# Kernel tuning notes

Measured on AMD Instinct MI355X. Metric: run time of the kernel, lower is better.

The kernel has to match this reference:

```python
import jax, jax.numpy as jnp
import numpy as np

K_NN = 3
EPS = 1e-8
MASK_THRESH = 0.5


def _three_nn_interpolate(pts, known, feats):
    """pts: (B,N,3), known: (B,M,3), feats: (B,M,C) -> (B,N,C).
    Squared-distance 3-NN + inverse-distance weighted interpolation
    (pointnet2 three_nn / three_interpolate semantics)."""
    # (B,N,M) squared euclidean distances
    d2 = (jnp.sum(pts * pts, -1)[:, :, None]
          + jnp.sum(known * known, -1)[:, None, :]
          - 2.0 * jnp.einsum('bnd,bmd->bnm', pts, known))
    neg_d, idx = jax.lax.top_k(-d2, K_NN)          # (B,N,3)
    dist = jnp.maximum(-neg_d, 0.0)                # squared dists, clamp fp error
    dist_recip = 1.0 / (dist + EPS)
    weight = dist_recip / jnp.sum(dist_recip, -1, keepdims=True)  # (B,N,3)
    b_idx = jnp.arange(pts.shape[0])[:, None, None]
    gathered = feats[b_idx, idx]                   # (B,N,3,C)
    return jnp.sum(weight[..., None] * gathered, axis=2)  # (B,N,C)


def setup_inputs() -> dict:
    key = jax.random.key(0)
    ks = jax.random.split(key, 10)
    B, N, C = 4, 8192, 32
    M2, M3, M4, Mm = 8192, 4096, 2048, 4096
    sc = 10.0  # spread coords over a realistic metric range
    return {
        'points_mean': jax.random.normal(ks[0], (B, N, 3)) * sc,
        'known2': jax.random.normal(ks[1], (B, M2, 3)) * sc,
        'feats2': jax.random.normal(ks[2], (B, M2, C)),
        'known3': jax.random.normal(ks[3], (B, M3, 3)) * sc,
        'feats3': jax.random.normal(ks[4], (B, M3, C)),
        'known4': jax.random.normal(ks[5], (B, M4, 3)) * sc,
        'feats4': jax.random.normal(ks[6], (B, M4, C)),
        'match_points': jax.random.normal(ks[7], (B, Mm, 3)) * sc,
        'w_fc': jax.random.normal(ks[8], (64, 96)) * 0.1,
        'w_cls': jax.random.normal(ks[9], (1, 64)) * 0.1,
    }


def reference(points_mean, known2, feats2, known3, feats3, known4, feats4,
              match_points, w_fc, w_cls):
    p0 = _three_nn_interpolate(points_mean, known2, feats2)  # (B,N,32)
    p1 = _three_nn_interpolate(points_mean, known3, feats3)
    p2 = _three_nn_interpolate(points_mean, known4, feats4)
    pointwise = jnp.concatenate([p0, p1, p2], axis=-1) @ w_fc.T  # (B,N,64)
    pred_hm = pointwise @ w_cls.T                                 # (B,N,1)
    # GT mask: min distance to match points < 0.5 m
    d2 = (jnp.sum(points_mean * points_mean, -1)[:, :, None]
          + jnp.sum(match_points * match_points, -1)[:, None, :]
          - 2.0 * jnp.einsum('bnd,bmd->bnm', points_mean, match_points))
    min_d = jnp.sqrt(jnp.maximum(jnp.min(d2, axis=-1), 0.0))      # (B,N)
    gt_hm = (min_d < MASK_THRESH).astype(jnp.float32)
    return pred_hm, gt_hm
```

## Files before the change

### kernel.cpp

```cpp
#include <hip/hip_runtime.h>

typedef unsigned int u32;
typedef unsigned long long u64;
typedef float f32x2 __attribute__((ext_vector_type(2)));

#define NB 4
#define NQ 8192
#define MARGIN 0.0625f
#define NBKT 4096

#define OFF_C0   0u
#define OFF_C1   524288u
#define OFF_C2   786432u
#define OFF_CMP  917504u
#define OFF_SKEY 1179648u
#define OFF_BOX  2031616u
#define WS_NEW2  2068480u
#define OFF_CM   917504u
#define WS_OLD   (512u*1024 + 256u*1024 + 128u*1024 + 512u*1024)

struct __align__(32) CP { f32x2 x, y, z, w; };
struct DM { double x, y, z, w; };

__device__ __forceinline__ f32x2 fma2(f32x2 a, f32x2 b, f32x2 c) {
  return __builtin_elementwise_fma(a, b, c);
}

__device__ __forceinline__ float wmaxf(float v) {
#pragma unroll
  for (int o = 32; o; o >>= 1) v = fmaxf(v, __shfl_xor(v, o));
  return v;
}
__device__ __forceinline__ float wminf(float v) {
#pragma unroll
  for (int o = 32; o; o >>= 1) v = fminf(v, __shfl_xor(v, o));
  return v;
}

__device__ __forceinline__ void lexins(double& e0d, double& e1d, double& e2d,
                                       int& e0i, int& e1i, int& e2i,
                                       double d, int i) {
  if (d < e2d || (d == e2d && i < e2i)) {
    if (d < e0d || (d == e0d && i < e0i)) {
      e2d = e1d; e2i = e1i; e1d = e0d; e1i = e0i; e0d = d; e0i = i;
    } else if (d < e1d || (d == e1d && i < e1i)) {
      e2d = e1d; e2i = e1i; e1d = d; e1i = i;
    } else {
      e2d = d; e2i = i;
    }
  }
}

__device__ __forceinline__ void ins4(float kv, u32 idx,
                                     float& k0, float& k1, float& k2, float& k3,
                                     u32& i0, u32& i1, u32& i2, u32& i3) {
  if (kv < k3) {
    bool lt0 = kv < k0, lt1 = kv < k1, lt2 = kv < k2;
    k3 = lt2 ? k2 : kv;               i3 = lt2 ? i2 : idx;
    k2 = lt2 ? (lt1 ? k1 : kv) : k2;  i2 = lt2 ? (lt1 ? i1 : idx) : i2;
    k1 = lt1 ? (lt0 ? k0 : kv) : k1;  i1 = lt1 ? (lt0 ? i0 : idx) : i1;
    k0 = lt0 ? kv : k0;               i0 = lt0 ? idx : i0;
  }
}

__device__ __forceinline__ u32 spread10(u32 v) {
  v &= 0x3FFu;
  v = (v | (v << 16)) & 0x030000FFu;
  v = (v | (v << 8))  & 0x0300F00Fu;
  v = (v | (v << 4))  & 0x030C30C3u;
  v = (v | (v << 2))  & 0x09249249u;
  return v;
}
__device__ __forceinline__ u32 morton30(float x, float y, float z) {
  int xi = (int)((x + 64.f) * 8.f);
  int yi = (int)((y + 64.f) * 8.f);
  int zi = (int)((z + 64.f) * 8.f);
  xi = min(max(xi, 0), 1023); yi = min(max(yi, 0), 1023); zi = min(max(zi, 0), 1023);
  return spread10((u32)xi) | (spread10((u32)yi) << 1) | (spread10((u32)zi) << 2);
}

__device__ __forceinline__ size_t skey_abase(int arr) {
  return (arr == 0) ? 0 : (arr == 1) ? 32768 : (arr == 2) ? 49152
        : (arr == 3) ? 57344 : 73728;
}

__global__ __launch_bounds__(1024) void prep_csort(
    const float* __restrict__ k2p, const float* __restrict__ k3p,
    const float* __restrict__ k4p, const float* __restrict__ mmp,
    const float* __restrict__ pts, u64* __restrict__ skey) {
  __shared__ u32 hist[NBKT];
  const int arr = blockIdx.x, b = blockIdx.y, tid = threadIdx.x;
  const float* src = (arr == 0) ? k2p : (arr == 1) ? k3p : (arr == 2) ? k4p
                      : (arr == 3) ? mmp : pts;
  const int n = (arr == 0) ? 8192 : (arr == 1) ? 4096 : (arr == 2) ? 2048
                 : (arr == 3) ? 4096 : 8192;
  const float* sb = src + (size_t)b * n * 3;
  u64* skb = skey + skey_abase(arr) + (size_t)b * n;

  for (int i = tid; i < NBKT; i += 1024) hist[i] = 0;
  __syncthreads();
  for (int i = tid; i < n; i += 1024) {
    u32 k = morton30(sb[3 * i], sb[3 * i + 1], sb[3 * i + 2]);
    atomicAdd(&hist[k >> 18], 1u);
  }
  __syncthreads();
  for (int d = 1; d < NBKT; d <<= 1) {
    for (int i = tid; i < NBKT / (2 * d); i += 1024) {
      int idx = (2 * i + 2) * d - 1;
      hist[idx] += hist[idx - d];
    }
    __syncthreads();
  }
  if (tid == 0) hist[NBKT - 1] = 0;
  __syncthreads();
  for (int d = NBKT >> 1; d >= 1; d >>= 1) {
    for (int i = tid; i < NBKT / (2 * d); i += 1024) {
      int idx = (2 * i + 2) * d - 1;
      u32 t = hist[idx - d];
      hist[idx - d] = hist[idx];
      hist[idx] += t;
    }
    __syncthreads();
  }
  for (int i = tid; i < n; i += 1024) {
    u32 k = morton30(sb[3 * i], sb[3 * i + 1], sb[3 * i + 2]);
    u32 pos = atomicAdd(&hist[k >> 18], 1u);
    skb[pos] = ((u64)k << 32) | (u32)i;
  }
}

__global__ __launch_bounds__(512) void refine_emit(
    const float* __restrict__ k2p, const float* __restrict__ k3p,
    const float* __restrict__ k4p, const float* __restrict__ mmp,
    const float* __restrict__ pts, u64* __restrict__ skey,
    CP* __restrict__ c0, CP* __restrict__ c1, CP* __restrict__ c2,
    CP* __restrict__ cmp, float* __restrict__ boxes) {
  __shared__ u64 ex[512];
  const int widx = blockIdx.x, b = blockIdx.y, tid = threadIdx.x;
  int arr, win;
  if (widx < 16)      { arr = 0; win = widx; }
  else if (widx < 24) { arr = 1; win = widx - 16; }
  else if (widx < 28) { arr = 2; win = widx - 24; }
  else if (widx < 36) { arr = 3; win = widx - 28; }
  else                { arr = 4; win = widx - 36; }
  const float* src = (arr == 0) ? k2p : (arr == 1) ? k3p : (arr == 2) ? k4p
                      : (arr == 3) ? mmp : pts;
  const int n = (arr == 0) ? 8192 : (arr == 1) ? 4096 : (arr == 2) ? 2048
                 : (arr == 3) ? 4096 : 8192;
  u64* skb = skey + skey_abase(arr) + (size_t)b * n;
  const int e = win * 512 + tid;
  u64 v = skb[e];

  for (int k = 2; k <= 512; k <<= 1) {
    for (int j = k >> 1; j > 0; j >>= 1) {
      u64 w;
      if (j < 64) {
        w = __shfl_xor(v, j);
      } else {
        __syncthreads();
        ex[tid] = v;
        __syncthreads();
        w = ex[tid ^ j];
      }
      bool up = (tid & k) == 0;
      bool lower = (tid & j) == 0;
      v = (up == lower) ? (v < w ? v : w) : (v < w ? w : v);
    }
  }
  skb[e] = v;
  if (arr == 4) return;

  u32 p = (u32)v;
  const float* sb = src + (size_t)b * n * 3;
  float x = sb[3 * p], y = sb[3 * p + 1], z = sb[3 * p + 2];
  {
    CP* dst = (arr == 0) ? c0 : (arr == 1) ? c1 : (arr == 2) ? c2 : cmp;
    float* df = (float*)(dst + (size_t)b * (n >> 1) + (e >> 1));
    int sl = e & 1;
    df[sl]     = x;
    df[2 + sl] = y;
    df[4 + sl] = z;
    df[6 + sl] = fmaf(z, z, fmaf(y, y, x * x));
  }
  float xlo = x, xhi = x, ylo = y, yhi = y, zlo = z, zhi = z;
#pragma unroll
  for (int off = 1; off < 64; off <<= 1) {
    xlo = fminf(xlo, __shfl_xor(xlo, off)); xhi = fmaxf(xhi, __shfl_xor(xhi, off));
    ylo = fminf(ylo, __shfl_xor(ylo, off)); yhi = fmaxf(yhi, __shfl_xor(yhi, off));
    zlo = fminf(zlo, __shfl_xor(zlo, off)); zhi = fmaxf(zhi, __shfl_xor(zhi, off));
  }
  if ((tid & 63) == 0) {
    const int nG = n >> 6, g = e >> 6;
    const int boff = (arr == 0) ? 0 : (arr == 1) ? 512 : (arr == 2) ? 768 : 896;
    float* bx = boxes + ((size_t)boff + (size_t)b * nG + g) * 8;
    bx[0] = xlo; bx[1] = xhi; bx[2] = ylo; bx[3] = yhi; bx[4] = zlo; bx[5] = zhi;
    bx[6] = 0.f; bx[7] = 0.f;
  }
}

__device__ __forceinline__ void scan_pairs16(
    const CP* __restrict__ cg, u32 ebase,
    f32x2 mx2, f32x2 my2, f32x2 mz2,
    float& k0, float& k1, float& k2, float& k3,
    u32& i0, u32& i1, u32& i2, u32& i3) {
#pragma unroll 4
  for (int gg = 0; gg < 16; gg += 4) {
    f32x2 key[4];
#pragma unroll
    for (int u = 0; u < 4; ++u) {
      CP c = cg[gg + u];
      key[u] = fma2(mx2, c.x, fma2(my2, c.y, fma2(mz2, c.z, c.w)));
    }
#pragma unroll
    for (int u = 0; u < 4; ++u) {
      float ka = key[u].x, kb = key[u].y;
      if (fminf(ka, kb) < k3) {
        u32 ib = ebase + (u32)((gg + u) * 2);
        ins4(ka, ib,     k0, k1, k2, k3, i0, i1, i2, i3);
        ins4(kb, ib + 1, k0, k1, k2, k3, i0, i1, i2, i3);
      }
    }
  }
}

struct Smem5 {
  float  qx[32], qy[32], qz[32];
  double qdx[32], qdy[32], qdz[32], qn[32];
  u32    oq[32];
  u32    di[3][32][4][4];
  double mmin[32][8];
  float  wv[96];
  float  wq[32][9];
  u32    iq[32][9];
  float  contrib[32][9];
  float4 stage[4][2][64];
};

__global__ __launch_bounds__(256, 4) void fused_sorted4(
    const float* __restrict__ pts,
    const float* __restrict__ f2, const float* __restrict__ f3,
    const float* __restrict__ f4,
    const float* __restrict__ wfc, const float* __restrict__ wcls,
    const CP* __restrict__ c0, const CP* __restrict__ c1,
    const CP* __restrict__ c2, const CP* __restrict__ cmp,
    const u64* __restrict__ skey, const float* __restrict__ boxes,
    float* __restrict__ out) {
  __shared__ Smem5 s;
  const int tid = threadIdx.x;
  const int b = blockIdx.y;
  const int tile = blockIdx.x;
  const int lane = tid & 63;
  const int q = tid & 31;
  const int h = (tid >> 5) & 1;
  const int wid = __builtin_amdgcn_readfirstlane(tid >> 6);

  if (tid < 32) {
    u64 kv = skey[73728 + (size_t)b * NQ + tile * 32 + tid];
    u32 p = (u32)kv;
    const float* pb = pts + (size_t)b * NQ * 3;
    float x = pb[3 * p], y = pb[3 * p + 1], z = pb[3 * p + 2];
    s.qx[tid] = x; s.qy[tid] = y; s.qz[tid] = z; s.oq[tid] = p;
    double dx = (double)x, dy = (double)y, dz = (double)z;
    s.qdx[tid] = dx; s.qdy[tid] = dy; s.qdz[tid] = dz;
    s.qn[tid] = (dx * dx + dy * dy) + dz * dz;
  } else if (tid < 128) {
    int t = tid - 32;
    float acc = 0.f;
    for (int j = 0; j < 64; ++j) acc += wcls[j] * wfc[j * 96 + t];
    s.wv[t] = acc;
  }
  __syncthreads();

  const float qx = s.qx[q], qy = s.qy[q], qz = s.qz[q];
  const float qnf = fmaf(qz, qz, fmaf(qy, qy, qx * qx));
  const float fm2x = -2.0f * qx, fm2y = -2.0f * qy, fm2z = -2.0f * qz;
  const double qdx = s.qdx[q], qdy = s.qdy[q], qdz = s.qdz[q], qn = s.qn[q];
  const f32x2 mx2 = {fm2x, fm2x}, my2 = {fm2y, fm2y}, mz2 = {fm2z, fm2z};

  const float txlo = wminf(qx), txhi = wmaxf(qx);
  const float tylo = wminf(qy), tyhi = wmaxf(qy);
  const float tzlo = wminf(qz), tzhi = wmaxf(qz);

  auto boxS = [&](const float* bxb, int gl) -> float {
    const float4* bp = (const float4*)(bxb + (size_t)gl * 8);
    float4 blo = bp[0], bhi = bp[1];
    float dx = fmaxf(fmaxf(blo.x - txhi, txlo - blo.y), 0.f);
    float dy = fmaxf(fmaxf(blo.z - tyhi, tylo - blo.w), 0.f);
    float dz = fmaxf(fmaxf(bhi.x - tzhi, tzlo - bhi.y), 0.f);
    return fmaf(dx, dx, fmaf(dy, dy, dz * dz));
  };

  {
    int lvl, part, gl;
    bool valid = true;
    if (wid < 2)      { lvl = 0; part = wid * 2 + h; gl = wid + 2 * lane; }
    else if (wid == 2){ lvl = 1; part = h;           gl = lane; }
    else              { lvl = 2; part = h;           gl = lane & 31; valid = lane < 32; }
    const int M = 8192 >> lvl;
    const int nG = M >> 6;
    const CP* c4 = ((lvl == 0) ? c0 : ((lvl == 1) ? c1 : c2)) + (((size_t)b * M) >> 1);
    const float* bxb = boxes +
        (size_t)(((lvl == 0) ? 0 : ((lvl == 1) ? 512 : 768)) + b * nG) * 8;

    float Ss = valid ? boxS(bxb, gl) : __builtin_inff();
    u32 gs = (u32)gl;
#pragma unroll
    for (int k = 2; k <= 64; k <<= 1) {
#pragma unroll
      for (int j = k >> 1; j > 0; j >>= 1) {
        float So = __shfl_xor(Ss, j);
        u32  go = __shfl_xor(gs, j);
        bool up = ((lane & k) == 0) == ((lane & j) == 0);
        bool take = up ? (So < Ss) : (So > Ss);
        if (take) { Ss = So; gs = go; }
      }
    }

    float k0 = __builtin_inff(), k1 = k0, k2 = k0, k3 = k0;
    u32 i0 = 0, i1 = 0, i2 = 0, i3 = 0;
    float Bmax = __builtin_inff();

    int i = 1, cur = 0, gcur = -1;
    float4 v;
    {
      float S0 = __shfl(Ss, 0);
      if (S0 < Bmax) { gcur = (int)__shfl(gs, 0);
                       v = ((const float4*)(c4 + (size_t)gcur * 32))[lane]; }
    }
    while (gcur >= 0) {
      s.stage[wid][cur][lane] = v;
      int gn = -1;
      if (i < 64) {
        float Sn = __shfl(Ss, i);
        if (Sn < Bmax) { gn = (int)__shfl(gs, i);
                         v = ((const float4*)(c4 + (size_t)gn * 32))[lane]; ++i; }
      }
      const CP* sg = (const CP*)&s.stage[wid][cur][0];
      scan_pairs16(sg + h * 16, (u32)(gcur * 64 + h * 32),
                   mx2, my2, mz2, k0, k1, k2, k3, i0, i1, i2, i3);
      Bmax = wmaxf(qnf + k3) + MARGIN;
      if (gn >= 0) {
        float Sg = __shfl(Ss, i - 1);
        if (Sg >= Bmax) gn = -1;
      }
      gcur = gn; cur ^= 1;
    }

    s.di[lvl][q][part][0] = i0; s.di[lvl][q][part][1] = i1;
    s.di[lvl][q][part][2] = i2; s.di[lvl][q][part][3] = i3;
  }

  {
    const CP* cmb = cmp + (size_t)b * 2048;
    const float* bxb = boxes + (size_t)(896 + b * 64) * 8;
    int glm = wid + 4 * (lane & 15);
    float Sm = (lane < 16) ? boxS(bxb, glm) : __builtin_inff();
    u64 bal = __ballot(Sm < 0.26f);
    double dmin = __builtin_inf();
    while (bal) {
      int bp = __builtin_ctzll(bal); bal &= bal - 1;
      int g = __shfl(glm, bp);
      const CP* cg = cmb + g * 32 + h * 16;
#pragma unroll 4
      for (int p = 0; p < 16; ++p) {
        CP c = cg[p];
        f32x2 key = fma2(mx2, c.x, fma2(my2, c.y, fma2(mz2, c.z, c.w)));
        if (fminf(key.x, key.y) + qnf < 0.252f) {
          {
            double x = (double)c.x.x, y = (double)c.y.x, z = (double)c.z.x;
            double kn2 = (x * x + y * y) + z * z;
            double dot = (qdx * x + qdy * y) + qdz * z;
            dmin = fmin(dmin, (qn + kn2) - 2.0 * dot);
          }
          {
            double x = (double)c.x.y, y = (double)c.y.y, z = (double)c.z.y;
            double kn2 = (x * x + y * y) + z * z;
            double dot = (qdx * x + qdy * y) + qdz * z;
            dmin = fmin(dmin, (qn + kn2) - 2.0 * dot);
          }
        }
      }
    }
    s.mmin[q][wid * 2 + h] = dmin;
  }
  __syncthreads();

  const int gqbase = b * NQ;
  if (tid < 96) {
    const int lvl = tid >> 5;
    const int qq = tid & 31;
    const int M  = 8192 >> lvl;
    const int np = (lvl == 0) ? 4 : 2;
    const CP* c4 = ((lvl == 0) ? c0 : ((lvl == 1) ? c1 : c2)) + (((size_t)b * M) >> 1);
    const u64* skl = skey + ((lvl == 0) ? 0 : (lvl == 1) ? 32768 : 49152)
                     + (size_t)b * M;
    const double tqdx = s.qdx[qq], tqdy = s.qdy[qq], tqdz = s.qdz[qq], tqn = s.qn[qq];
    double e0 = __builtin_inf(), e1 = e0, e2 = e0;
    int j0 = 0, j1 = 0, j2 = 0;
    for (int hh = 0; hh < np; ++hh) {
#pragma unroll
      for (int r = 0; r < 4; ++r) {
        int sidx = (int)s.di[lvl][qq][hh][r];
        CP cc = c4[sidx >> 1];
        bool hi = sidx & 1;
        double x = (double)(hi ? cc.x.y : cc.x.x);
        double y = (double)(hi ? cc.y.y : cc.y.x);
        double z = (double)(hi ? cc.z.y : cc.z.x);
        int orig = (int)(u32)skl[sidx];
        double kn2 = (x * x + y * y) + z * z;
        double dot = (tqdx * x + tqdy * y) + tqdz * z;
        double d2 = (tqn + kn2) - 2.0 * dot;
        lexins(e0, e1, e2, j0, j1, j2, d2, orig);
      }
    }
    double d0 = fmax(e0, 0.0), d1 = fmax(e1, 0.0), d2v = fmax(e2, 0.0);
    double r0 = 1.0 / (d0 + 1e-8);
    double r1 = 1.0 / (d1 + 1e-8);
    double r2 = 1.0 / (d2v + 1e-8);
    double sum = (r0 + r1) + r2;
    s.wq[qq][lvl * 3 + 0] = (float)(r0 / sum); s.iq[qq][lvl * 3 + 0] = (u32)j0;
    s.wq[qq][lvl * 3 + 1] = (float)(r1 / sum); s.iq[qq][lvl * 3 + 1] = (u32)j1;
    s.wq[qq][lvl * 3 + 2] = (float)(r2 / sum); s.iq[qq][lvl * 3 + 2] = (u32)j2;
  } else if (tid < 128) {
    const int qq = tid - 96;
    double dm = s.mmin[qq][0];
#pragma unroll
    for (int p = 1; p < 8; ++p) dm = fmin(dm, s.mmin[qq][p]);
    out[NB * NQ + gqbase + (int)s.oq[qq]] = (dm < 0.25) ? 1.0f : 0.0f;
  }
  __syncthreads();

  for (int item = tid; item < 288; item += 256) {
    const int qq = item & 31, j = item >> 5;
    const int lvl = j / 3;
    const float* fp = (lvl == 0) ? f2 : ((lvl == 1) ? f3 : f4);
    const int M = 8192 >> lvl;
    const float4* row = (const float4*)(fp + ((size_t)b * M + s.iq[qq][j]) * 32);
    const float* wvp = s.wv + lvl * 32;
    float acc = 0.f;
#pragma unroll
    for (int v = 0; v < 8; ++v) {
      float4 r = row[v];
      acc += wvp[4 * v] * r.x + wvp[4 * v + 1] * r.y
           + wvp[4 * v + 2] * r.z + wvp[4 * v + 3] * r.w;
    }
    s.contrib[qq][j] = s.wq[qq][j] * acc;
  }
  __syncthreads();
  if (tid < 32) {
    const float* c = s.contrib[tid];
    float l0 = (c[0] + c[1]) + c[2];
    float l1 = (c[3] + c[4]) + c[5];
    float l2 = (c[6] + c[7]) + c[8];
    out[gqbase + (int)s.oq[tid]] = (l0 + l1) + l2;
  }
}

__global__ __launch_bounds__(256) void prep_kernel(
    const float* __restrict__ k2p, const float* __restrict__ k3p,
    const float* __restrict__ k4p, const float* __restrict__ mmp,
    CP* __restrict__ c0, CP* __restrict__ c1,
    CP* __restrict__ c2, DM* __restrict__ cm) {
  int r = blockIdx.y;
  int i = blockIdx.x * 256 + threadIdx.x;
  if (r < 3) {
    const float* src = (r == 0) ? k2p : ((r == 1) ? k3p : k4p);
    CP* dst = (r == 0) ? c0 : ((r == 1) ? c1 : c2);
    int pairs = (r == 0) ? NB * 4096 : ((r == 1) ? NB * 2048 : NB * 1024);
    if (i >= pairs) return;
    const float* p = src + (size_t)i * 6;
    float x0 = p[0], y0 = p[1], z0 = p[2];
    float x1 = p[3], y1 = p[4], z1 = p[5];
    CP c;
    c.x = f32x2{x0, x1}; c.y = f32x2{y0, y1}; c.z = f32x2{z0, z1};
    c.w = f32x2{fmaf(z0, z0, fmaf(y0, y0, x0 * x0)),
                fmaf(z1, z1, fmaf(y1, y1, x1 * x1))};
    dst[i] = c;
  } else {
    if (i >= NB * 4096) return;
    double x = (double)mmp[3 * i], y = (double)mmp[3 * i + 1], z = (double)mmp[3 * i + 2];
    DM d = {x, y, z, fma(z, z, fma(y, y, x * x))};
    cm[i] = d;
  }
}

template <bool PREP>
__device__ __forceinline__ void scan_nn(
    const CP* __restrict__ cp, const float* __restrict__ raw,
    int gstart, int L, float m2x, float m2y, float m2z,
    float* kk, u32* ii) {
  float k0 = __builtin_inff(), k1 = k0, k2 = k0, k3 = k0;
  u32 i0 = 0, i1 = 0, i2 = 0, i3 = 0;
  if (PREP) {
    const f32x2 mx2 = {m2x, m2x}, my2 = {m2y, m2y}, mz2 = {m2z, m2z};
    const int G = L >> 1;
#pragma unroll 2
    for (int g = 0; g < G; g += 4) {
      f32x2 key[4];
#pragma unroll
      for (int u = 0; u < 4; ++u) {
        CP c = cp[g + u];
        key[u] = fma2(mx2, c.x, fma2(my2, c.y, fma2(mz2, c.z, c.w)));
      }
#pragma unroll
      for (int u = 0; u < 4; ++u) {
        float ka = key[u].x, kb = key[u].y;
        if (fminf(ka, kb) < k3) {
          u32 ib = (u32)(gstart + 2 * (g + u));
          ins4(ka, ib,     k0, k1, k2, k3, i0, i1, i2, i3);
          ins4(kb, ib + 1, k0, k1, k2, k3, i0, i1, i2, i3);
        }
      }
    }
  } else {
    for (int j = 0; j < L; j += 8) {
      float key[8];
#pragma unroll
      for (int u = 0; u < 8; ++u) {
        const float* p = raw + (size_t)(gstart + j + u) * 3;
        float x = p[0], y = p[1], z = p[2];
        float n2 = fmaf(z, z, fmaf(y, y, x * x));
        key[u] = fmaf(m2x, x, fmaf(m2y, y, fmaf(m2z, z, n2)));
      }
#pragma unroll
      for (int u = 0; u < 8; ++u)
        ins4(key[u], (u32)(gstart + j + u), k0, k1, k2, k3, i0, i1, i2, i3);
    }
  }
  kk[0] = k0; kk[1] = k1; kk[2] = k2; kk[3] = k3;
  ii[0] = i0; ii[1] = i1; ii[2] = i2; ii[3] = i3;
}

template <bool PREP>
__device__ __forceinline__ double scan_mask(
    const DM* __restrict__ c8, const float* __restrict__ raw,
    int gstart, int L, double m2x, double m2y, double m2z) {
  double smin = __builtin_inf();
  if (PREP) {
    for (int j = 0; j < L; j += 8) {
      double sv[8];
#pragma unroll
      for (int u = 0; u < 8; ++u) {
        DM c = c8[gstart + j + u];
        sv[u] = fma(m2x, c.x, fma(m2y, c.y, fma(m2z, c.z, c.w)));
      }
      double m01 = fmin(sv[0], sv[1]), m23 = fmin(sv[2], sv[3]);
      double m45 = fmin(sv[4], sv[5]), m67 = fmin(sv[6], sv[7]);
      smin = fmin(smin, fmin(fmin(m01, m23), fmin(m45, m67)));
    }
  } else {
    for (int j = 0; j < L; j += 4) {
#pragma unroll
      for (int u = 0; u < 4; ++u) {
        const float* p = raw + (size_t)(gstart + j + u) * 3;
        double x = (double)p[0], y = (double)p[1], z = (double)p[2];
        double kn = fma(z, z, fma(y, y, x * x));
        smin = fmin(smin, fma(m2x, x, fma(m2y, y, fma(m2z, z, kn))));
      }
    }
  }
  return smin;
}

struct Smem {
  float  qx[64], qy[64], qz[64];
  double qdx[64], qdy[64], qdz[64], qn[64];
  float  dk[3][64][4][4];
  u32    di[3][64][4][4];
  double mmin[64][8];
  float  wv[96];
  float  part[64][3];
};

template <bool PREP>
__global__ __launch_bounds__(512, 2) void fused_kernel(
    const float* __restrict__ pts,
    const float* __restrict__ k2p, const float* __restrict__ f2,
    const float* __restrict__ k3p, const float* __restrict__ f3,
    const float* __restrict__ k4p, const float* __restrict__ f4,
    const float* __restrict__ mmp,
    const float* __restrict__ wfc, const float* __restrict__ wcls,
    const CP* __restrict__ c0, const CP* __restrict__ c1,
    const CP* __restrict__ c2, const DM* __restrict__ cm,
    float* __restrict__ out) {
  __shared__ Smem s;
  const int tid = threadIdx.x;
  const int b = blockIdx.y;
  const int q0 = blockIdx.x * 64;
  const int qloc = tid & 63;
  const int wid = __builtin_amdgcn_readfirstlane(tid >> 6);

  if (tid < 64) {
    int gq = b * NQ + q0 + tid;
    float x = pts[3 * gq], y = pts[3 * gq + 1], z = pts[3 * gq + 2];
    s.qx[tid] = x; s.qy[tid] = y; s.qz[tid] = z;
    double dx = (double)x, dy = (double)y, dz = (double)z;
    s.qdx[tid] = dx; s.qdy[tid] = dy; s.qdz[tid] = dz;
    s.qn[tid] = (dx * dx + dy * dy) + dz * dz;
  } else if (tid < 160) {
    int t = tid - 64;
    float acc = 0.f;
    for (int j = 0; j < 64; ++j) acc += wcls[j] * wfc[j * 96 + t];
    s.wv[t] = acc;
  }
  __syncthreads();

  const float fm2x = -2.0f * s.qx[qloc];
  const float fm2y = -2.0f * s.qy[qloc];
  const float fm2z = -2.0f * s.qz[qloc];
  const double dm2x = -2.0 * s.qdx[qloc];
  const double dm2y = -2.0 * s.qdy[qloc];
  const double dm2z = -2.0 * s.qdz[qloc];

  {
    int lvl, prt, gstart, glen;
    if (wid < 4)      { lvl = 0; prt = wid;     gstart = wid * 2048;       glen = 2048; }
    else if (wid < 6) { lvl = 1; prt = wid - 4; gstart = (wid - 4) * 2048; glen = 2048; }
    else              { lvl = 2; prt = wid - 6; gstart = (wid - 6) * 1024; glen = 1024; }
    const CP* c4 = (lvl == 0) ? c0 : ((lvl == 1) ? c1 : c2);
    const float* raw = (lvl == 0) ? k2p : ((lvl == 1) ? k3p : k4p);
    const int      M = (lvl == 0) ? 8192 : ((lvl == 1) ? 4096 : 2048);
    float kk[4]; u32 ii[4];
    scan_nn<PREP>(c4 + (PREP ? (((size_t)b * M + gstart) >> 1) : 0),
                  raw + (size_t)b * M * 3,
                  gstart, glen, fm2x, fm2y, fm2z, kk, ii);
#pragma unroll
    for (int r = 0; r < 4; ++r) {
      s.dk[lvl][qloc][prt][r] = kk[r];
      s.di[lvl][qloc][prt][r] = ii[r];
    }
    int mstart, mlen;
    if (wid < 6) { mstart = wid * 256; mlen = 256; }
    else         { mstart = 1536 + (wid - 6) * 1280; mlen = 1280; }
    s.mmin[qloc][wid] = scan_mask<PREP>(cm + (PREP ? (size_t)b * 4096 : 0),
                                        mmp + (size_t)b * 4096 * 3,
                                        mstart, mlen, dm2x, dm2y, dm2z);
  }
  __syncthreads();

  const int gqbase = b * NQ + q0;
  if (tid < 192) {
    const int lvl = __builtin_amdgcn_readfirstlane(tid >> 6);
    const int q = tid & 63;
    const float* kp = (lvl == 0) ? k2p : ((lvl == 1) ? k3p : k4p);
    const int    M  = (lvl == 0) ? 8192 : ((lvl == 1) ? 4096 : 2048);
    const int    np = (lvl == 0) ? 4 : 2;
    const double qdx = s.qdx[q], qdy = s.qdy[q], qdz = s.qdz[q], qn = s.qn[q];
    double e0 = __builtin_inf(), e1 = e0, e2 = e0;
    int i0 = 0, i1 = 0, i2 = 0;
    for (int h = 0; h < np; ++h) {
#pragma unroll
      for (int r = 0; r < 4; ++r) {
        int idx = (int)s.di[lvl][q][h][r];
        const float* c = kp + ((size_t)b * M + idx) * 3;
        double x = (double)c[0], y = (double)c[1], z = (double)c[2];
        double kn2 = (x * x + y * y) + z * z;
        double dot = (qdx * x + qdy * y) + qdz * z;
        double d2 = (qn + kn2) - 2.0 * dot;
        lexins(e0, e1, e2, i0, i1, i2, d2, idx);
      }
    }
    double d0 = fmax(e0, 0.0), d1 = fmax(e1, 0.0), d2v = fmax(e2, 0.0);
    double r0 = 1.0 / (d0 + 1e-8);
    double r1 = 1.0 / (d1 + 1e-8);
    double r2 = 1.0 / (d2v + 1e-8);
    double sum = (r0 + r1) + r2;
    float wa = (float)(r0 / sum), wb = (float)(r1 / sum), wc = (float)(r2 / sum);
    const float* fp = (lvl == 0) ? f2 : ((lvl == 1) ? f3 : f4);
    const float* g0 = fp + ((size_t)b * M + i0) * 32;
    const float* g1 = fp + ((size_t)b * M + i1) * 32;
    const float* g2 = fp + ((size_t)b * M + i2) * 32;
    float acc = 0.f;
#pragma unroll
    for (int wd = 0; wd < 32; ++wd) {
      float v = (wa * g0[wd] + wb * g1[wd]) + wc * g2[wd];
      acc += s.wv[lvl * 32 + wd] * v;
    }
    s.part[q][lvl] = acc;
  } else if (tid < 256) {
    const int q = tid - 192;
    double sm = s.mmin[q][0];
#pragma unroll
    for (int p = 1; p < 8; ++p) sm = fmin(sm, s.mmin[q][p]);
    double dm = s.qn[q] + sm;
    out[NB * NQ + gqbase + q] = (dm < 0.25) ? 1.0f : 0.0f;
  }
  __syncthreads();
  if (tid < 64) {
    float pred = (s.part[tid][0] + s.part[tid][1]) + s.part[tid][2];
    out[gqbase + tid] = pred;
  }
}

extern "C" void kernel_launch(void* const* d_in, const int* in_sizes, int n_in,
                              void* d_out, int out_size, void* d_ws, size_t ws_size,
                              hipStream_t stream) {
  const float* pts    = (const float*)d_in[0];
  const float* known2 = (const float*)d_in[1];
  const float* feats2 = (const float*)d_in[2];
  const float* known3 = (const float*)d_in[3];
  const float* feats3 = (const float*)d_in[4];
  const float* known4 = (const float*)d_in[5];
  const float* feats4 = (const float*)d_in[6];
  const float* match  = (const float*)d_in[7];
  const float* wfc    = (const float*)d_in[8];
  const float* wcls   = (const float*)d_in[9];

  char* ws = (char*)d_ws;
  CP* c0 = (CP*)(ws + OFF_C0);
  CP* c1 = (CP*)(ws + OFF_C1);
  CP* c2 = (CP*)(ws + OFF_C2);

  if (ws_size >= WS_NEW2) {
    CP* cmp = (CP*)(ws + OFF_CMP);
    u64* skey = (u64*)(ws + OFF_SKEY);
    float* boxes = (float*)(ws + OFF_BOX);
    hipLaunchKernelGGL(prep_csort, dim3(5, NB), dim3(1024), 0, stream,
                       known2, known3, known4, match, pts, skey);
    hipLaunchKernelGGL(refine_emit, dim3(52, NB), dim3(512), 0, stream,
                       known2, known3, known4, match, pts, skey,
                       c0, c1, c2, cmp, boxes);
    hipLaunchKernelGGL(fused_sorted4, dim3(NQ / 32, NB), dim3(256), 0, stream,
                       pts, feats2, feats3, feats4, wfc, wcls,
                       c0, c1, c2, cmp, skey, boxes, (float*)d_out);
  } else if (ws_size >= WS_OLD) {
    DM* cm = (DM*)(ws + OFF_CM);
    hipLaunchKernelGGL(prep_kernel, dim3(64, 4), dim3(256), 0, stream,
                       known2, known3, known4, match, c0, c1, c2, cm);
    hipLaunchKernelGGL(HIP_KERNEL_NAME(fused_kernel<true>), dim3(NQ / 64, NB),
                       dim3(512), 0, stream, pts, known2, feats2, known3, feats3,
                       known4, feats4, match, wfc, wcls, c0, c1, c2, cm,
                       (float*)d_out);
  } else {
    DM* cm = (DM*)(ws + OFF_CM);
    hipLaunchKernelGGL(HIP_KERNEL_NAME(fused_kernel<false>), dim3(NQ / 64, NB),
                       dim3(512), 0, stream, pts, known2, feats2, known3, feats3,
                       known4, feats4, match, wfc, wcls, c0, c1, c2, cm,
                       (float*)d_out);
  }
}
```

Before: 276.3 us.

## Share kNN pruning bound across waves via LDS atomicMin and rebalance wave work

```diff
diff --git a/kernel.cpp b/kernel.cpp
--- a/kernel.cpp
+++ b/kernel.cpp
@@ -29,11 +29,6 @@
 __device__ __forceinline__ float wmaxf(float v) {
 #pragma unroll
   for (int o = 32; o; o >>= 1) v = fmaxf(v, __shfl_xor(v, o));
-  return v;
-}
-__device__ __forceinline__ float wminf(float v) {
-#pragma unroll
-  for (int o = 32; o; o >>= 1) v = fminf(v, __shfl_xor(v, o));
   return v;
 }
 
@@ -89,7 +84,9 @@
     const float* __restrict__ k4p, const float* __restrict__ mmp,
     const float* __restrict__ pts, u64* __restrict__ skey) {
   __shared__ u32 hist[NBKT];
+  __shared__ u32 wsum[16];
   const int arr = blockIdx.x, b = blockIdx.y, tid = threadIdx.x;
+  const int lane = tid & 63, wv = tid >> 6;
   const float* src = (arr == 0) ? k2p : (arr == 1) ? k3p : (arr == 2) ? k4p
                       : (arr == 3) ? mmp : pts;
   const int n = (arr == 0) ? 8192 : (arr == 1) ? 4096 : (arr == 2) ? 2048
@@ -104,24 +101,33 @@
     atomicAdd(&hist[k >> 18], 1u);
   }
   __syncthreads();
-  for (int d = 1; d < NBKT; d <<= 1) {
-    for (int i = tid; i < NBKT / (2 * d); i += 1024) {
-      int idx = (2 * i + 2) * d - 1;
-      hist[idx] += hist[idx - d];
-    }
-    __syncthreads();
-  }
-  if (tid == 0) hist[NBKT - 1] = 0;
-  __syncthreads();
-  for (int d = NBKT >> 1; d >= 1; d >>= 1) {
-    for (int i = tid; i < NBKT / (2 * d); i += 1024) {
-      int idx = (2 * i + 2) * d - 1;
-      u32 t = hist[idx - d];
-      hist[idx - d] = hist[idx];
-      hist[idx] += t;
-    }
-    __syncthreads();
-  }
+  u32 h0 = hist[4 * tid], h1 = hist[4 * tid + 1];
+  u32 h2 = hist[4 * tid + 2], h3 = hist[4 * tid + 3];
+  u32 s4 = h0 + h1 + h2 + h3;
+  u32 inc = s4;
+#pragma unroll
+  for (int o = 1; o < 64; o <<= 1) {
+    u32 t = __shfl_up(inc, o);
+    if (lane >= o) inc += t;
+  }
+  if (lane == 63) wsum[wv] = inc;
+  __syncthreads();
+  if (tid < 16) {
+    u32 v = wsum[tid], in = v;
+#pragma unroll
+    for (int o = 1; o < 16; o <<= 1) {
+      u32 t = __shfl_up(in, o);
+      if (tid >= o) in += t;
+    }
+    wsum[tid] = in - v;
+  }
+  __syncthreads();
+  u32 excl = wsum[wv] + (inc - s4);
+  hist[4 * tid]     = excl;
+  hist[4 * tid + 1] = excl + h0;
+  hist[4 * tid + 2] = excl + h0 + h1;
+  hist[4 * tid + 3] = excl + h0 + h1 + h2;
+  __syncthreads();
   for (int i = tid; i < n; i += 1024) {
     u32 k = morton30(sb[3 * i], sb[3 * i + 1], sb[3 * i + 2]);
     u32 pos = atomicAdd(&hist[k >> 18], 1u);
@@ -223,12 +229,13 @@
   }
 }
 
-struct Smem5 {
+struct Smem6 {
   float  qx[32], qy[32], qz[32];
   double qdx[32], qdy[32], qdz[32], qn[32];
   u32    oq[32];
+  int    ibnd[3][32];
   u32    di[3][32][4][4];
-  double mmin[32][8];
+  double mmin[32][2];
   float  wv[96];
   float  wq[32][9];
   u32    iq[32][9];
@@ -236,7 +243,7 @@
   float4 stage[4][2][64];
 };
 
-__global__ __launch_bounds__(256, 4) void fused_sorted4(
+__global__ __launch_bounds__(256, 4) void fused_sorted5(
     const float* __restrict__ pts,
     const float* __restrict__ f2, const float* __restrict__ f3,
     const float* __restrict__ f4,
@@ -245,7 +252,7 @@
     const CP* __restrict__ c2, const CP* __restrict__ cmp,
     const u64* __restrict__ skey, const float* __restrict__ boxes,
     float* __restrict__ out) {
-  __shared__ Smem5 s;
+  __shared__ Smem6 s;
   const int tid = threadIdx.x;
   const int b = blockIdx.y;
   const int tile = blockIdx.x;
@@ -268,6 +275,8 @@
     float acc = 0.f;
     for (int j = 0; j < 64; ++j) acc += wcls[j] * wfc[j * 96 + t];
     s.wv[t] = acc;
+  } else if (tid < 224) {
+    ((int*)s.ibnd)[tid - 128] = 0x7F800000;
   }
   __syncthreads();
 
@@ -277,9 +286,9 @@
   const double qdx = s.qdx[q], qdy = s.qdy[q], qdz = s.qdz[q], qn = s.qn[q];
   const f32x2 mx2 = {fm2x, fm2x}, my2 = {fm2y, fm2y}, mz2 = {fm2z, fm2z};
 
-  const float txlo = wminf(qx), txhi = wmaxf(qx);
-  const float tylo = wminf(qy), tyhi = wmaxf(qy);
-  const float tzlo = wminf(qz), tzhi = wmaxf(qz);
+  const float txlo = -wmaxf(-qx), txhi = wmaxf(qx);
+  const float tylo = -wmaxf(-qy), tyhi = wmaxf(qy);
+  const float tzlo = -wmaxf(-qz), tzhi = wmaxf(qz);
 
   auto boxS = [&](const float* bxb, int gl) -> float {
     const float4* bp = (const float4*)(bxb + (size_t)gl * 8);
@@ -291,11 +300,13 @@
   };
 
   {
-    int lvl, part, gl;
+    int lvl, pbase, gl;
     bool valid = true;
-    if (wid < 2)      { lvl = 0; part = wid * 2 + h; gl = wid + 2 * lane; }
-    else if (wid == 2){ lvl = 1; part = h;           gl = lane; }
-    else              { lvl = 2; part = h;           gl = lane & 31; valid = lane < 32; }
+    if (wid == 0)      { lvl = 0; pbase = 0; gl = 2 * lane; }
+    else if (wid == 3) { lvl = 0; pbase = 2; gl = 2 * lane + 1; }
+    else if (wid == 1) { lvl = 1; pbase = 0; gl = lane; }
+    else               { lvl = 2; pbase = 0; gl = lane & 31; valid = lane < 32; }
+    const int part = pbase + h;
     const int M = 8192 >> lvl;
     const int nG = M >> 6;
     const CP* c4 = ((lvl == 0) ? c0 : ((lvl == 1) ? c1 : c2)) + (((size_t)b * M) >> 1);
@@ -318,6 +329,7 @@
 
     float k0 = __builtin_inff(), k1 = k0, k2 = k0, k3 = k0;
     u32 i0 = 0, i1 = 0, i2 = 0, i3 = 0;
+    volatile int* bq = &s.ibnd[lvl][q];
     float Bmax = __builtin_inff();
 
     int i = 1, cur = 0, gcur = -1;
@@ -338,7 +350,12 @@
       const CP* sg = (const CP*)&s.stage[wid][cur][0];
       scan_pairs16(sg + h * 16, (u32)(gcur * 64 + h * 32),
                    mx2, my2, mz2, k0, k1, k2, k3, i0, i1, i2, i3);
-      Bmax = wmaxf(qnf + k3) + MARGIN;
+      {
+        float b0 = __shfl_xor(k0, 32), b1 = __shfl_xor(k1, 32), b2v = __shfl_xor(k2, 32);
+        float u2 = fminf(fminf(k2, b2v), fminf(fmaxf(k1, b0), fmaxf(k0, b1)));
+        if (h == 0) atomicMin((int*)bq, __float_as_int(qnf + u2));
+      }
+      Bmax = wmaxf(__int_as_float(*bq)) + MARGIN;
       if (gn >= 0) {
         float Sg = __shfl(Ss, i - 1);
         if (Sg >= Bmax) gn = -1;
@@ -350,16 +367,14 @@
     s.di[lvl][q][part][2] = i2; s.di[lvl][q][part][3] = i3;
   }
 
-  {
+  if (wid == 2) {
     const CP* cmb = cmp + (size_t)b * 2048;
     const float* bxb = boxes + (size_t)(896 + b * 64) * 8;
-    int glm = wid + 4 * (lane & 15);
-    float Sm = (lane < 16) ? boxS(bxb, glm) : __builtin_inff();
+    float Sm = boxS(bxb, lane);
     u64 bal = __ballot(Sm < 0.26f);
     double dmin = __builtin_inf();
     while (bal) {
-      int bp = __builtin_ctzll(bal); bal &= bal - 1;
-      int g = __shfl(glm, bp);
+      int g = __builtin_ctzll(bal); bal &= bal - 1;
       const CP* cg = cmb + g * 32 + h * 16;
 #pragma unroll 4
       for (int p = 0; p < 16; ++p) {
@@ -381,7 +396,7 @@
         }
       }
     }
-    s.mmin[q][wid * 2 + h] = dmin;
+    s.mmin[q][h] = dmin;
   }
   __syncthreads();
 
@@ -423,9 +438,7 @@
     s.wq[qq][lvl * 3 + 2] = (float)(r2 / sum); s.iq[qq][lvl * 3 + 2] = (u32)j2;
   } else if (tid < 128) {
     const int qq = tid - 96;
-    double dm = s.mmin[qq][0];
-#pragma unroll
-    for (int p = 1; p < 8; ++p) dm = fmin(dm, s.mmin[qq][p]);
+    double dm = fmin(s.mmin[qq][0], s.mmin[qq][1]);
     out[NB * NQ + gqbase + (int)s.oq[qq]] = (dm < 0.25) ? 1.0f : 0.0f;
   }
   __syncthreads();
@@ -720,7 +733,7 @@
     hipLaunchKernelGGL(refine_emit, dim3(52, NB), dim3(512), 0, stream,
                        known2, known3, known4, match, pts, skey,
                        c0, c1, c2, cmp, boxes);
-    hipLaunchKernelGGL(fused_sorted4, dim3(NQ / 32, NB), dim3(256), 0, stream,
+    hipLaunchKernelGGL(fused_sorted5, dim3(NQ / 32, NB), dim3(256), 0, stream,
                        pts, feats2, feats3, feats4, wfc, wcls,
                        c0, c1, c2, cmp, skey, boxes, (float*)d_out);
   } else if (ws_size >= WS_OLD) {
```

Measured after the change: 315.9 us. +14.3%, slower.
